# Kernel optimization log

Measured on AMD Instinct MI355X. Metric: run time of the kernel, lower is better.

## Reference

```python
import jax, jax.numpy as jnp
import numpy as np

K = 12  # kNN neighbors (includes self, as in PyG knn(x, x, k))
EPS = 1e-5


def bn(h, g, b):
    # Training-mode BatchNorm over all axes except the last (feature) axis.
    ax = tuple(range(h.ndim - 1))
    m = h.mean(axis=ax, keepdims=True)
    v = h.var(axis=ax, keepdims=True)  # biased variance, as BN uses
    return g * (h - m) * jax.lax.rsqrt(v + EPS) + b


def edge_conv(x, W1, b1, g, be, W2, b2):
    # x: [B, N, C] -> [B, N, H]. Dynamic kNN graph in feature space per graph.
    d2 = jnp.sum(x * x, axis=-1)                                  # [B, N]
    dist = d2[:, :, None] + d2[:, None, :] - 2.0 * jnp.einsum('bic,bjc->bij', x, x)
    _, idx = jax.lax.top_k(-dist, K)                              # [B, N, K]
    xj = jnp.take_along_axis(x[:, None, :, :], idx[:, :, :, None], axis=2)  # [B,N,K,C]
    xi = jnp.broadcast_to(x[:, :, None, :], xj.shape)
    e = jnp.concatenate([xi, xj - xi], axis=-1)                   # [B,N,K,2C]
    h = jax.nn.relu(bn(jnp.einsum('bnkc,ch->bnkh', e, W1) + b1, g, be))
    h = jnp.einsum('bnkh,ho->bnko', h, W2) + b2
    return h.mean(axis=2)                                         # mean aggr over K


def setup_inputs() -> dict:
    key = jax.random.key(0)
    ks = jax.random.split(key, 8)
    B, N, C, H, Hf, O = 32, 1024, 3, 64, 32, 2
    s = 0.1
    return {
        'x': jax.random.normal(ks[0], (B, N, C), jnp.float32),
        'w0a': jax.random.normal(ks[1], (2 * C, H), jnp.float32) * s,
        'b0a': jnp.zeros((H,), jnp.float32),
        'g0': jnp.ones((H,), jnp.float32),
        'be0': jnp.zeros((H,), jnp.float32),
        'w0b': jax.random.normal(ks[2], (H, H), jnp.float32) * s,
        'b0b': jnp.zeros((H,), jnp.float32),
        'wa': jax.random.normal(ks[3], (3, 2 * H, H), jnp.float32) * s,
        'ba': jnp.zeros((3, H), jnp.float32),
        'ga': jnp.ones((3, H), jnp.float32),
        'bea': jnp.zeros((3, H), jnp.float32),
        'wb': jax.random.normal(ks[4], (3, H, H), jnp.float32) * s,
        'bb': jnp.zeros((3, H), jnp.float32),
        'wf1': jax.random.normal(ks[5], (H, Hf), jnp.float32) * s,
        'bf1': jnp.zeros((Hf,), jnp.float32),
        'gf': jnp.ones((Hf,), jnp.float32),
        'bef': jnp.zeros((Hf,), jnp.float32),
        'wf2': jax.random.normal(ks[6], (Hf, O), jnp.float32) * s,
        'bf2': jnp.zeros((O,), jnp.float32),
    }


def reference(x, w0a, b0a, g0, be0, w0b, b0b, wa, ba, ga, bea, wb, bb,
              wf1, bf1, gf, bef, wf2, bf2):
    # Layer 0: input channels = 3
    h = edge_conv(x, w0a, b0a, g0, be0, w0b, b0b)
    # Layers 1..3: input channels = hidden
    for i in range(3):
        h = edge_conv(h, wa[i], ba[i], ga[i], bea[i], wb[i], bb[i])
    pooled = h.mean(axis=1)  # global_mean_pool over nodes -> [B, H]
    z = jax.nn.relu(bn(pooled @ wf1 + bf1, gf, bef))
    return z @ wf2 + bf2     # [B, 2]
```

## Files before the change

### kernel.cpp

```cpp
#include <hip/hip_runtime.h>
#include <cstddef>

#define BATCH 32
#define NPTS  1024
#define K_NN  12
#define HID   64
#define BN_EPS 1e-5f

typedef short bf16x8 __attribute__((ext_vector_type(8)));
typedef float f32x4 __attribute__((ext_vector_type(4)));

template<int C>
__global__ __launch_bounds__(256) void d2_kernel(const float* __restrict__ x,
                                                 float* __restrict__ d2) {
  int gid = blockIdx.x * 256 + threadIdx.x;
  const float* xp = x + (size_t)gid * C;
  float s = 0.f;
#pragma unroll
  for (int c = 0; c < C; ++c) { float v = xp[c]; s = fmaf(v, v, s); }
  d2[gid] = s;
}

__device__ __forceinline__ unsigned long long dkey(float dval, int j) {
  int di = __float_as_int(dval);
  unsigned m = (unsigned)(di >> 31) | 0x80000000u;
  unsigned u = (unsigned)di ^ m;
  return ((unsigned long long)u << 32) | (unsigned)j;
}

__device__ __forceinline__ void cas_u64(unsigned long long &a, unsigned long long &b) {
  unsigned long long x = a, y = b;
  bool c = y < x;
  a = c ? y : x;
  b = c ? x : y;
}

__device__ __forceinline__ void sort16_u64(unsigned long long (&k)[16]) {
  cas_u64(k[0],k[1]);  cas_u64(k[2],k[3]);  cas_u64(k[4],k[5]);  cas_u64(k[6],k[7]);
  cas_u64(k[8],k[9]);  cas_u64(k[10],k[11]); cas_u64(k[12],k[13]); cas_u64(k[14],k[15]);
  cas_u64(k[0],k[2]);  cas_u64(k[1],k[3]);  cas_u64(k[4],k[6]);  cas_u64(k[5],k[7]);
  cas_u64(k[8],k[10]); cas_u64(k[9],k[11]); cas_u64(k[12],k[14]); cas_u64(k[13],k[15]);
  cas_u64(k[1],k[2]);  cas_u64(k[5],k[6]);  cas_u64(k[9],k[10]); cas_u64(k[13],k[14]);
  cas_u64(k[0],k[4]);  cas_u64(k[1],k[5]);  cas_u64(k[2],k[6]);  cas_u64(k[3],k[7]);
  cas_u64(k[8],k[12]); cas_u64(k[9],k[13]); cas_u64(k[10],k[14]); cas_u64(k[11],k[15]);
  cas_u64(k[2],k[4]);  cas_u64(k[3],k[5]);  cas_u64(k[10],k[12]); cas_u64(k[11],k[13]);
  cas_u64(k[1],k[2]);  cas_u64(k[3],k[4]);  cas_u64(k[5],k[6]);
  cas_u64(k[9],k[10]); cas_u64(k[11],k[12]); cas_u64(k[13],k[14]);
  cas_u64(k[0],k[8]);  cas_u64(k[1],k[9]);  cas_u64(k[2],k[10]); cas_u64(k[3],k[11]);
  cas_u64(k[4],k[12]); cas_u64(k[5],k[13]); cas_u64(k[6],k[14]); cas_u64(k[7],k[15]);
  cas_u64(k[4],k[8]);  cas_u64(k[5],k[9]);  cas_u64(k[6],k[10]); cas_u64(k[7],k[11]);
  cas_u64(k[2],k[4]);  cas_u64(k[3],k[5]);  cas_u64(k[6],k[8]);  cas_u64(k[7],k[9]);
  cas_u64(k[10],k[12]); cas_u64(k[11],k[13]);
  cas_u64(k[1],k[2]);  cas_u64(k[3],k[4]);  cas_u64(k[5],k[6]);  cas_u64(k[7],k[8]);
  cas_u64(k[9],k[10]); cas_u64(k[11],k[12]); cas_u64(k[13],k[14]);
}

__device__ __forceinline__ void merge12_u64(unsigned long long (&L)[12],
                                            const unsigned long long* S) {
#pragma unroll
  for (int i = 0; i < 12; ++i) {
    unsigned long long s = S[11 - i];
    L[i] = L[i] < s ? L[i] : s;
  }
  cas_u64(L[0],L[8]);  cas_u64(L[1],L[9]);  cas_u64(L[2],L[10]); cas_u64(L[3],L[11]);
  cas_u64(L[4],L[8]);  cas_u64(L[5],L[9]);  cas_u64(L[6],L[10]); cas_u64(L[7],L[11]);
  cas_u64(L[0],L[2]);  cas_u64(L[1],L[3]);  cas_u64(L[4],L[6]);  cas_u64(L[5],L[7]);
  cas_u64(L[8],L[10]); cas_u64(L[9],L[11]);
  cas_u64(L[0],L[1]);  cas_u64(L[2],L[3]);  cas_u64(L[4],L[5]);  cas_u64(L[6],L[7]);
  cas_u64(L[8],L[9]);  cas_u64(L[10],L[11]);
}

__global__ __launch_bounds__(512, 2) void knn64_mfma_kernel(
    const unsigned short* __restrict__ xh, const unsigned short* __restrict__ xm,
    const unsigned short* __restrict__ xl, const float* __restrict__ d2,
    int* __restrict__ idx,
    const float* __restrict__ hxi, const float* __restrict__ hxj,
    float* __restrict__ partial) {
  const int b    = blockIdx.y;
  const int lane = threadIdx.x & 63;
  const int wv_u = __builtin_amdgcn_readfirstlane(threadIdx.x >> 6);
  const int i0   = blockIdx.x * 64;
  const size_t bbase = (size_t)b * NPTS;
  const float* d2b = d2 + bbase;

  constexpr int NE = 8 * K_NN;
  __shared__ __align__(16) char smem[60416];
  unsigned short* alds = (unsigned short*)smem;
  float* slab = (float*)(smem + 25600 + wv_u * 4352);
  unsigned long long* lk = (unsigned long long*)smem;
  int* jlds = (int*)(smem + 49664);
  float* red1 = (float*)smem;
  float* red2 = (float*)(smem + 2048);

  const int qr = lane >> 4;
  const int lr = lane & 15;

  for (int it = threadIdx.x; it < 1536; it += 512) {
    const int row = it / 24, rem = it % 24, pl = rem >> 3, seg = rem & 7;
    const unsigned short* src = (pl == 0) ? xh : ((pl == 1) ? xm : xl);
    *(bf16x8*)(alds + row * 200 + pl * 64 + seg * 8) =
        *(const bf16x8*)(src + (bbase + i0 + row) * HID + seg * 8);
  }
  __syncthreads();

  unsigned long long L[K_NN];
#pragma unroll
  for (int k = 0; k < K_NN; ++k) L[k] = ~0ULL;

  const int j0 = wv_u * 128;

  bf16x8 Bh0, Bh1, Bm0, Bm1, Bl0, Bl1;
  {
    const size_t brow = (bbase + j0 + lr) * HID;
    Bh0 = *(const bf16x8*)(xh + brow + 0  + qr * 8);
    Bh1 = *(const bf16x8*)(xh + brow + 32 + qr * 8);
    Bm0 = *(const bf16x8*)(xm + brow + 0  + qr * 8);
    Bm1 = *(const bf16x8*)(xm + brow + 32 + qr * 8);
    Bl0 = *(const bf16x8*)(xl + brow + 0  + qr * 8);
    Bl1 = *(const bf16x8*)(xl + brow + 32 + qr * 8);
  }

#pragma unroll 1
  for (int chunk = 0; chunk < 8; ++chunk) {
    const int jb = j0 + chunk * 16;
    const bf16x8 bh0 = Bh0, bh1 = Bh1, bm0 = Bm0, bm1 = Bm1, bl0 = Bl0, bl1 = Bl1;

    f32x4 acc[4];
#pragma unroll
    for (int isub = 0; isub < 4; ++isub) acc[isub] = f32x4{0.f, 0.f, 0.f, 0.f};

#pragma unroll
    for (int isub = 0; isub < 4; ++isub) {
      const int ar = (isub * 16 + lr) * 200;
      bf16x8 Ah0 = *(const bf16x8*)(alds + ar + 0   + qr * 8);
      bf16x8 Ah1 = *(const bf16x8*)(alds + ar + 32  + qr * 8);
      bf16x8 Am0 = *(const bf16x8*)(alds + ar + 64  + qr * 8);
      bf16x8 Am1 = *(const bf16x8*)(alds + ar + 96  + qr * 8);
      bf16x8 Al0 = *(const bf16x8*)(alds + ar + 128 + qr * 8);
      bf16x8 Al1 = *(const bf16x8*)(alds + ar + 160 + qr * 8);
      f32x4 a = acc[isub];
      a = __builtin_amdgcn_mfma_f32_16x16x32_bf16(Ah0, bh0, a, 0, 0, 0);
      a = __builtin_amdgcn_mfma_f32_16x16x32_bf16(Ah1, bh1, a, 0, 0, 0);
      a = __builtin_amdgcn_mfma_f32_16x16x32_bf16(Ah0, bm0, a, 0, 0, 0);
      a = __builtin_amdgcn_mfma_f32_16x16x32_bf16(Ah1, bm1, a, 0, 0, 0);
      a = __builtin_amdgcn_mfma_f32_16x16x32_bf16(Am0, bh0, a, 0, 0, 0);
      a = __builtin_amdgcn_mfma_f32_16x16x32_bf16(Am1, bh1, a, 0, 0, 0);
      a = __builtin_amdgcn_mfma_f32_16x16x32_bf16(Ah0, bl0, a, 0, 0, 0);
      a = __builtin_amdgcn_mfma_f32_16x16x32_bf16(Ah1, bl1, a, 0, 0, 0);
      a = __builtin_amdgcn_mfma_f32_16x16x32_bf16(Al0, bh0, a, 0, 0, 0);
      a = __builtin_amdgcn_mfma_f32_16x16x32_bf16(Al1, bh1, a, 0, 0, 0);
      a = __builtin_amdgcn_mfma_f32_16x16x32_bf16(Am0, bm0, a, 0, 0, 0);
      a = __builtin_amdgcn_mfma_f32_16x16x32_bf16(Am1, bm1, a, 0, 0, 0);
      acc[isub] = a;
    }

    if (chunk < 7) {
      const size_t nrow = (bbase + jb + 16 + lr) * HID;
      Bh0 = *(const bf16x8*)(xh + nrow + 0  + qr * 8);
      Bh1 = *(const bf16x8*)(xh + nrow + 32 + qr * 8);
      Bm0 = *(const bf16x8*)(xm + nrow + 0  + qr * 8);
      Bm1 = *(const bf16x8*)(xm + nrow + 32 + qr * 8);
      Bl0 = *(const bf16x8*)(xl + nrow + 0  + qr * 8);
      Bl1 = *(const bf16x8*)(xl + nrow + 32 + qr * 8);
    }

#pragma unroll
    for (int isub = 0; isub < 4; ++isub)
#pragma unroll
      for (int r = 0; r < 4; ++r)
        slab[(isub * 16 + qr * 4 + r) * 17 + lr] = acc[isub][r];

    unsigned long long S[16];
#pragma unroll
    for (int jj = 0; jj < 16; ++jj) {
      const int j = jb + jj;
      const float dot = slab[lane * 17 + jj];
      const float dval = fmaf(-2.f, dot, d2b[j]);
      S[jj] = dkey(dval, j);
    }
    sort16_u64(S);
    merge12_u64(L, S);
  }

  __syncthreads();
#pragma unroll
  for (int k = 0; k < K_NN; ++k)
    lk[lane * (NE + 1) + wv_u * K_NN + k] = L[k];
  __syncthreads();

  unsigned long long Lm[K_NN];
  if (wv_u < 2) {
    if (wv_u == 0) {
#pragma unroll
      for (int k = 0; k < K_NN; ++k) Lm[k] = L[k];
    } else {
#pragma unroll
      for (int k = 0; k < K_NN; ++k) Lm[k] = lk[lane * (NE + 1) + 4 * K_NN + k];
    }
#pragma unroll 1
    for (int w = 1; w < 4; ++w) {
      unsigned long long M[K_NN];
#pragma unroll
      for (int k = 0; k < K_NN; ++k)
        M[k] = lk[lane * (NE + 1) + (wv_u * 4 + w) * K_NN + k];
      merge12_u64(Lm, M);
    }
  }
  __syncthreads();
  if (wv_u == 1) {
#pragma unroll
    for (int k = 0; k < K_NN; ++k) lk[lane * (NE + 1) + 4 * K_NN + k] = Lm[k];
  }
  __syncthreads();
  if (wv_u == 0) {
    unsigned long long M[K_NN];
#pragma unroll
    for (int k = 0; k < K_NN; ++k) M[k] = lk[lane * (NE + 1) + 4 * K_NN + k];
    merge12_u64(Lm, M);
    int* op = idx + ((size_t)b * NPTS + i0 + lane) * K_NN;
#pragma unroll
    for (int k = 0; k < K_NN; ++k) {
      int jv = (int)(unsigned)(Lm[k] & 0xFFFFFFFFu);
      op[k] = jv;
      jlds[lane * K_NN + k] = jv;
    }
  }
  __syncthreads();

  {
    const float* hxib = hxi + (bbase + i0) * HID;
    const float* hxjb = hxj + bbase * HID;
    float s1 = 0.f, s2 = 0.f;
#pragma unroll 1
    for (int t = 0; t < 8; ++t) {
      const int nl = wv_u * 8 + t;
      const float hv = hxib[(size_t)nl * HID + lane];
      int jj[K_NN];
#pragma unroll
      for (int k = 0; k < K_NN; ++k) jj[k] = jlds[nl * K_NN + k];
      float v[K_NN];
#pragma unroll
      for (int k = 0; k < K_NN; ++k) v[k] = hxjb[(size_t)jj[k] * HID + lane];
#pragma unroll
      for (int k = 0; k < K_NN; ++k) {
        float h = hv + v[k];
        s1 += h;
        s2 = fmaf(h, h, s2);
      }
    }
    red1[wv_u * HID + lane] = s1;
    red2[wv_u * HID + lane] = s2;
  }
  __syncthreads();
  if (threadIdx.x < 128) {
    const int f = threadIdx.x & 63;
    const float* r = (threadIdx.x < 64) ? red1 : red2;
    float a = 0.f;
#pragma unroll
    for (int w = 0; w < 8; ++w) a += r[w * HID + f];
    partial[((size_t)b * 16 + blockIdx.x) * 128 + threadIdx.x] = a;
  }
}

__global__ __launch_bounds__(512, 2) void knn3_kernel(
    const float* __restrict__ x, const float* __restrict__ d2,
    int* __restrict__ idx,
    const float* __restrict__ hxi, const float* __restrict__ hxj,
    float* __restrict__ partial) {
  const int b    = blockIdx.y;
  const int lane = threadIdx.x & 63;
  const int wv_u = __builtin_amdgcn_readfirstlane(threadIdx.x >> 6);
  const int i0   = blockIdx.x * 64;
  const int i    = i0 + lane;
  const size_t bbase = (size_t)b * NPTS;
  const float* xb  = x  + bbase * 3;
  const float* d2b = d2 + bbase;

  constexpr int NE = 8 * K_NN;
  __shared__ __align__(16) char smem[53248];
  unsigned long long* lk = (unsigned long long*)smem;
  int* jlds = (int*)(smem + 49664);
  float* red1 = (float*)smem;
  float* red2 = (float*)(smem + 2048);

  float xi0 = xb[(size_t)i * 3 + 0];
  float xi1 = xb[(size_t)i * 3 + 1];
  float xi2v = xb[(size_t)i * 3 + 2];

  unsigned long long L[K_NN];
#pragma unroll
  for (int k = 0; k < K_NN; ++k) L[k] = ~0ULL;

  const int j0 = wv_u * 128;
#pragma unroll 1
  for (int ch = 0; ch < 8; ++ch) {
    unsigned long long S[16];
#pragma unroll
    for (int jj = 0; jj < 16; ++jj) {
      const int j = j0 + ch * 16 + jj;
      const float* xj = xb + (size_t)j * 3;
      const float d2j = d2b[j];
      float dot = fmaf(xi0, xj[0], 0.f);
      dot = fmaf(xi1, xj[1], dot);
      dot = fmaf(xi2v, xj[2], dot);
      S[jj] = dkey(fmaf(-2.f, dot, d2j), j);
    }
    sort16_u64(S);
    merge12_u64(L, S);
  }

#pragma unroll
  for (int k = 0; k < K_NN; ++k)
    lk[lane * (NE + 1) + wv_u * K_NN + k] = L[k];
  __syncthreads();

  unsigned long long Lm[K_NN];
  if (wv_u < 2) {
    if (wv_u == 0) {
#pragma unroll
      for (int k = 0; k < K_NN; ++k) Lm[k] = L[k];
    } else {
#pragma unroll
      for (int k = 0; k < K_NN; ++k) Lm[k] = lk[lane * (NE + 1) + 4 * K_NN + k];
    }
#pragma unroll 1
    for (int w = 1; w < 4; ++w) {
      unsigned long long M[K_NN];
#pragma unroll
      for (int k = 0; k < K_NN; ++k)
        M[k] = lk[lane * (NE + 1) + (wv_u * 4 + w) * K_NN + k];
      merge12_u64(Lm, M);
    }
  }
  __syncthreads();
  if (wv_u == 1) {
#pragma unroll
    for (int k = 0; k < K_NN; ++k) lk[lane * (NE + 1) + 4 * K_NN + k] = Lm[k];
  }
  __syncthreads();
  if (wv_u == 0) {
    unsigned long long M[K_NN];
#pragma unroll
    for (int k = 0; k < K_NN; ++k) M[k] = lk[lane * (NE + 1) + 4 * K_NN + k];
    merge12_u64(Lm, M);
    int* op = idx + ((size_t)b * NPTS + i0 + lane) * K_NN;
#pragma unroll
    for (int k = 0; k < K_NN; ++k) {
      int jv = (int)(unsigned)(Lm[k] & 0xFFFFFFFFu);
      op[k] = jv;
      jlds[lane * K_NN + k] = jv;
    }
  }
  __syncthreads();

  {
    const float* hxib = hxi + (bbase + i0) * HID;
    const float* hxjb2 = hxj + bbase * HID;
    float s1 = 0.f, s2 = 0.f;
#pragma unroll 1
    for (int t = 0; t < 8; ++t) {
      const int nl = wv_u * 8 + t;
      const float hv = hxib[(size_t)nl * HID + lane];
      int jj[K_NN];
#pragma unroll
      for (int k = 0; k < K_NN; ++k) jj[k] = jlds[nl * K_NN + k];
      float v[K_NN];
#pragma unroll
      for (int k = 0; k < K_NN; ++k) v[k] = hxjb2[(size_t)jj[k] * HID + lane];
#pragma unroll
      for (int k = 0; k < K_NN; ++k) {
        float h = hv + v[k];
        s1 += h;
        s2 = fmaf(h, h, s2);
      }
    }
    red1[wv_u * HID + lane] = s1;
    red2[wv_u * HID + lane] = s2;
  }
  __syncthreads();
  if (threadIdx.x < 128) {
    const int f = threadIdx.x & 63;
    const float* r = (threadIdx.x < 64) ? red1 : red2;
    float a = 0.f;
#pragma unroll
    for (int w = 0; w < 8; ++w) a += r[w * HID + f];
    partial[((size_t)b * 16 + blockIdx.x) * 128 + threadIdx.x] = a;
  }
}

__global__ __launch_bounds__(256) void rowgemm2_kernel(
    const float* __restrict__ X, const float* __restrict__ waL,
    const float* __restrict__ biasA,
    float* __restrict__ YA, float* __restrict__ YB) {
  __shared__ float wsa[HID * HID];
  __shared__ float wsb[HID * HID];
  for (int t = threadIdx.x; t < HID * HID; t += 256) {
    float wbv = waL[4096 + t];
    wsa[t] = waL[t] - wbv;
    wsb[t] = wbv;
  }
  __syncthreads();

  const int lane = threadIdx.x & 63;
  const int wv   = threadIdx.x >> 6;
  const int fq   = lane & 15;
  const int rg   = lane >> 4;
  const int r0   = blockIdx.x * 32 + wv * 8 + rg * 2;

  const float4* X4 = (const float4*)X;
  const float4* WA4 = (const float4*)wsa;
  const float4* WB4 = (const float4*)wsb;
  float aA0[4] = {0,0,0,0}, aA1[4] = {0,0,0,0};
  float aB0[4] = {0,0,0,0}, aB1[4] = {0,0,0,0};

#pragma unroll 2
  for (int cq = 0; cq < 16; ++cq) {
    float4 xa = X4[(size_t)r0 * 16 + cq];
    float4 xb_ = X4[(size_t)(r0 + 1) * 16 + cq];
    float ea[4] = {xa.x, xa.y, xa.z, xa.w};
    float eb[4] = {xb_.x, xb_.y, xb_.z, xb_.w};
#pragma unroll
    for (int d = 0; d < 4; ++d) {
      float4 wa4 = WA4[(cq * 4 + d) * 16 + fq];
      float4 wb4 = WB4[(cq * 4 + d) * 16 + fq];
      float wA[4] = {wa4.x, wa4.y, wa4.z, wa4.w};
      float wB[4] = {wb4.x, wb4.y, wb4.z, wb4.w};
#pragma unroll
      for (int k = 0; k < 4; ++k) {
        aA0[k] = fmaf(ea[d], wA[k], aA0[k]);
        aA1[k] = fmaf(eb[d], wA[k], aA1[k]);
        aB0[k] = fmaf(ea[d], wB[k], aB0[k]);
        aB1[k] = fmaf(eb[d], wB[k], aB1[k]);
      }
    }
  }
  float4 b4 = ((const float4*)biasA)[fq];
  float4 oA0{aA0[0] + b4.x, aA0[1] + b4.y, aA0[2] + b4.z, aA0[3] + b4.w};
  float4 oA1{aA1[0] + b4.x, aA1[1] + b4.y, aA1[2] + b4.z, aA1[3] + b4.w};
  float4 oB0{aB0[0], aB0[1], aB0[2], aB0[3]};
  float4 oB1{aB1[0], aB1[1], aB1[2], aB1[3]};
  ((float4*)YA)[(size_t)r0 * 16 + fq] = oA0;
  ((float4*)YA)[(size_t)(r0 + 1) * 16 + fq] = oA1;
  ((float4*)YB)[(size_t)r0 * 16 + fq] = oB0;
  ((float4*)YB)[(size_t)(r0 + 1) * 16 + fq] = oB1;
}

__global__ __launch_bounds__(256) void dual3_kernel(
    const float* __restrict__ x, const float* __restrict__ w0a,
    const float* __restrict__ b1,
    float* __restrict__ hxi, float* __restrict__ hxj) {
  __shared__ float Cs[3 * HID], Bs[3 * HID], bs[HID];
  for (int t = threadIdx.x; t < 3 * HID; t += 256) {
    float bv = w0a[192 + t];
    Cs[t] = w0a[t] - bv;
    Bs[t] = bv;
  }
  if (threadIdx.x < HID) bs[threadIdx.x] = b1[threadIdx.x];
  __syncthreads();

  const int lane = threadIdx.x & 63;
  const int wv   = __builtin_amdgcn_readfirstlane(threadIdx.x >> 6);
  const int node0 = blockIdx.x * 32;
#pragma unroll 1
  for (int it = 0; it < 8; ++it) {
    const int n = node0 + it * 4 + wv;
    const float* xr = x + (size_t)n * 3;
    float x0 = xr[0], x1 = xr[1], x2 = xr[2];
    float hi = bs[lane];
    hi = fmaf(x0, Cs[0 * HID + lane], hi);
    hi = fmaf(x1, Cs[1 * HID + lane], hi);
    hi = fmaf(x2, Cs[2 * HID + lane], hi);
    float hj = x0 * Bs[0 * HID + lane];
    hj = fmaf(x1, Bs[1 * HID + lane], hj);
    hj = fmaf(x2, Bs[2 * HID + lane], hj);
    hxi[(size_t)n * HID + lane] = hi;
    hxj[(size_t)n * HID + lane] = hj;
  }
}

__global__ __launch_bounds__(512) void bn_reduce_finalize_kernel(
    const float* __restrict__ g, const float* __restrict__ be,
    const float* __restrict__ partial, float* __restrict__ stats) {
  const int t   = threadIdx.x & 127;
  const int grp = threadIdx.x >> 7;
  float a0 = 0.f, a1 = 0.f, a2 = 0.f, a3 = 0.f;
  const int gb0 = grp * 128;
  for (int gb = gb0; gb < gb0 + 128; gb += 4) {
    a0 += partial[(size_t)(gb + 0) * 128 + t];
    a1 += partial[(size_t)(gb + 1) * 128 + t];
    a2 += partial[(size_t)(gb + 2) * 128 + t];
    a3 += partial[(size_t)(gb + 3) * 128 + t];
  }
  __shared__ float sm[4][128];
  sm[grp][t] = (a0 + a1) + (a2 + a3);
  __syncthreads();
  if (threadIdx.x < 128)
    sm[0][t] = (sm[0][t] + sm[1][t]) + (sm[2][t] + sm[3][t]);
  __syncthreads();
  if (threadIdx.x < HID) {
    const float inv_n = 1.f / (float)(BATCH * NPTS * K_NN);
    float m = sm[0][t] * inv_n;
    float v = sm[0][HID + t] * inv_n - m * m;
    float A = g[t] * rsqrtf(v + BN_EPS);
    stats[128 + t] = A;
    stats[192 + t] = be[t] - m * A;
  }
}

__global__ __launch_bounds__(256) void egapply_gemm_kernel(
    const int* __restrict__ idx, const float* __restrict__ hxi,
    const float* __restrict__ hxj, const float* __restrict__ stats,
    const float* __restrict__ W2, const float* __restrict__ b2,
    float* __restrict__ out, float* __restrict__ d2out,
    unsigned short* __restrict__ xsh, unsigned short* __restrict__ xsm,
    unsigned short* __restrict__ xsl) {
  __shared__ float w2s[HID * HID];
  __shared__ float red[32][HID];
  for (int t = threadIdx.x; t < HID * HID; t += 256) w2s[t] = W2[t];

  const int lane = threadIdx.x & 63;
  const int wv   = __builtin_amdgcn_readfirstlane(threadIdx.x >> 6);
  const int node0 = blockIdx.x * 32;
  const float A = stats[128 + lane], Bc = stats[192 + lane];

#pragma unroll 1
  for (int it = 0; it < 4; ++it) {
    const int n0 = node0 + it * 8 + wv;
    const int n1 = n0 + 4;
    const int bbase = (n0 >> 10) << 10;
    const int* ip0 = idx + (size_t)n0 * K_NN;
    const int* ip1 = idx + (size_t)n1 * K_NN;
    int j0[K_NN], j1[K_NN];
#pragma unroll
    for (int k = 0; k < K_NN; ++k) { j0[k] = ip0[k]; j1[k] = ip1[k]; }
    const float hv0 = hxi[(size_t)n0 * HID + lane];
    const float hv1 = hxi[(size_t)n1 * HID + lane];
    float v0[K_NN], v1[K_NN];
#pragma unroll
    for (int k = 0; k < K_NN; ++k) {
      v0[k] = hxj[(size_t)(bbase + j0[k]) * HID + lane];
      v1[k] = hxj[(size_t)(bbase + j1[k]) * HID + lane];
    }
    float a0 = 0.f, a1 = 0.f;
#pragma unroll
    for (int k = 0; k < K_NN; ++k) {
      a0 += fmaxf(fmaf(A, hv0 + v0[k], Bc), 0.f);
      a1 += fmaxf(fmaf(A, hv1 + v1[k], Bc), 0.f);
    }
    red[it * 8 + wv][lane] = a0;
    red[it * 8 + 4 + wv][lane] = a1;
  }
  __syncthreads();

  const float b2f = b2[lane];
  const float inv = 1.f / (float)K_NN;
#pragma unroll 2
  for (int p = 0; p < 8; ++p) {
    int rr = p * 4 + wv;
    float acc = 0.f;
#pragma unroll 8
    for (int h = 0; h < HID; ++h) acc = fmaf(red[rr][h], w2s[h * HID + lane], acc);
    float val = fmaf(acc, inv, b2f);
    const size_t o = (size_t)(node0 + rr) * HID + lane;
    out[o] = val;

    unsigned u = __float_as_uint(val);
    unsigned short hh = (unsigned short)((u + 0x7FFFu + ((u >> 16) & 1u)) >> 16);
    float r1 = val - __uint_as_float((unsigned)hh << 16);
    unsigned ur = __float_as_uint(r1);
    unsigned short mm = (unsigned short)((ur + 0x7FFFu + ((ur >> 16) & 1u)) >> 16);
    float r2 = r1 - __uint_as_float((unsigned)mm << 16);
    unsigned ur2 = __float_as_uint(r2);
    unsigned short ll = (unsigned short)((ur2 + 0x7FFFu + ((ur2 >> 16) & 1u)) >> 16);
    xsh[o] = hh; xsm[o] = mm; xsl[o] = ll;

    float sq = val * val;
#pragma unroll
    for (int off = 1; off < 64; off <<= 1) sq += __shfl_xor(sq, off, 64);
    if (lane == 0) d2out[node0 + rr] = sq;
  }
}

__global__ __launch_bounds__(256) void pool_kernel(const float* __restrict__ h,
                                                   float* __restrict__ pooled) {
  const int b = blockIdx.x;
  const int f = threadIdx.x & 63;
  const int gsz = threadIdx.x >> 6;
  __shared__ float red[4][HID];
  float s = 0.f;
  for (int n = gsz; n < NPTS; n += 4) s += h[((size_t)b * NPTS + n) * HID + f];
  red[gsz][f] = s;
  __syncthreads();
  if (threadIdx.x < HID)
    pooled[b * HID + f] = ((red[0][f] + red[1][f]) + (red[2][f] + red[3][f])) * (1.f / (float)NPTS);
}

__global__ __launch_bounds__(256) void head_kernel(const float* __restrict__ pooled,
    const float* __restrict__ wf1, const float* __restrict__ bf1,
    const float* __restrict__ gf, const float* __restrict__ bef,
    const float* __restrict__ wf2, const float* __restrict__ bf2,
    float* __restrict__ out) {
  __shared__ float pl[BATCH * HID];
  __shared__ float t[BATCH * 32];
  __shared__ float Ab[32], Bb[32];
  for (int i = threadIdx.x; i < BATCH * HID; i += 256) pl[i] = pooled[i];
  __syncthreads();
  for (int i = threadIdx.x; i < BATCH * 32; i += 256) {
    int s = i >> 5, f1 = i & 31;
    float acc = bf1[f1];
    for (int h = 0; h < HID; ++h) acc = fmaf(pl[s * HID + h], wf1[h * 32 + f1], acc);
    t[i] = acc;
  }
  __syncthreads();
  if (threadIdx.x < 32) {
    int f1 = threadIdx.x;
    float m = 0.f;
    for (int s = 0; s < BATCH; ++s) m += t[s * 32 + f1];
    m *= (1.f / (float)BATCH);
    float v = 0.f;
    for (int s = 0; s < BATCH; ++s) { float d = t[s * 32 + f1] - m; v = fmaf(d, d, v); }
    v *= (1.f / (float)BATCH);
    float A = gf[f1] * rsqrtf(v + BN_EPS);
    Ab[f1] = A; Bb[f1] = bef[f1] - m * A;
  }
  __syncthreads();
  for (int i = threadIdx.x; i < BATCH * 32; i += 256) {
    int f1 = i & 31;
    t[i] = fmaxf(fmaf(Ab[f1], t[i], Bb[f1]), 0.f);
  }
  __syncthreads();
  if (threadIdx.x < BATCH * 2) {
    int s = threadIdx.x >> 1, o = threadIdx.x & 1;
    float acc = bf2[o];
    for (int f1 = 0; f1 < 32; ++f1) acc = fmaf(t[s * 32 + f1], wf2[f1 * 2 + o], acc);
    out[s * 2 + o] = acc;
  }
}

extern "C" void kernel_launch(void* const* d_in, const int* in_sizes, int n_in,
                              void* d_out, int out_size, void* d_ws, size_t ws_size,
                              hipStream_t stream) {
  const float* x   = (const float*)d_in[0];
  const float* w0a = (const float*)d_in[1];
  const float* b0a = (const float*)d_in[2];
  const float* g0  = (const float*)d_in[3];
  const float* be0 = (const float*)d_in[4];
  const float* w0b = (const float*)d_in[5];
  const float* b0b = (const float*)d_in[6];
  const float* wa  = (const float*)d_in[7];
  const float* ba  = (const float*)d_in[8];
  const float* ga  = (const float*)d_in[9];
  const float* bea = (const float*)d_in[10];
  const float* wb  = (const float*)d_in[11];
  const float* bb  = (const float*)d_in[12];
  const float* wf1 = (const float*)d_in[13];
  const float* bf1 = (const float*)d_in[14];
  const float* gf  = (const float*)d_in[15];
  const float* bef = (const float*)d_in[16];
  const float* wf2 = (const float*)d_in[17];
  const float* bf2 = (const float*)d_in[18];

  float* ws = (float*)d_ws;
  const size_t HN = (size_t)BATCH * NPTS * HID;
  const size_t ROWS = (size_t)BATCH * NPTS;
  float* bufA    = ws;
  float* bufB    = bufA + HN;
  float* hxi     = bufB + HN;
  float* hxjb    = hxi + HN;
  int*   idxb    = (int*)(hxjb + HN);
  float* d2buf   = (float*)(idxb + ROWS * K_NN);
  float* stats   = d2buf + ROWS;
  float* partial = stats + 256;
  float* pooled  = partial + 1024 * 128;
  unsigned short* xsh = (unsigned short*)(pooled + 2048);
  unsigned short* xsm = xsh + HN;
  unsigned short* xsl = xsm + HN;

  d2_kernel<3><<<(int)(ROWS / 256), 256, 0, stream>>>(x, d2buf);
  dual3_kernel<<<1024, 256, 0, stream>>>(x, w0a, b0a, hxi, hxjb);
  knn3_kernel<<<dim3(16, BATCH), 512, 0, stream>>>(x, d2buf, idxb, hxi, hxjb, partial);
  bn_reduce_finalize_kernel<<<1, 512, 0, stream>>>(g0, be0, partial, stats);
  egapply_gemm_kernel<<<1024, 256, 0, stream>>>(idxb, hxi, hxjb, stats, w0b, b0b,
                                                bufA, d2buf, xsh, xsm, xsl);

  const float* cur = bufA;
  float* nxt = bufB;
  for (int i = 0; i < 3; ++i) {
    rowgemm2_kernel<<<(int)(ROWS / 32), 256, 0, stream>>>(cur, wa + (size_t)i * 8192,
                                                          ba + i * HID, hxi, hxjb);
    knn64_mfma_kernel<<<dim3(16, BATCH), 512, 0, stream>>>(xsh, xsm, xsl, d2buf, idxb,
                                                           hxi, hxjb, partial);
    bn_reduce_finalize_kernel<<<1, 512, 0, stream>>>(ga + i * HID, bea + i * HID, partial, stats);
    egapply_gemm_kernel<<<1024, 256, 0, stream>>>(idxb, hxi, hxjb, stats,
                                                  wb + (size_t)i * 4096, bb + i * HID,
                                                  nxt, d2buf, xsh, xsm, xsl);
    const float* t = cur; cur = nxt; nxt = (float*)t;
  }

  pool_kernel<<<BATCH, 256, 0, stream>>>(cur, pooled);
  head_kernel<<<1, 256, 0, stream>>>(pooled, wf1, bf1, gf, bef, wf2, bf2, (float*)d_out);
}
```

Before: 580.0 us.

## Software-pipeline kNN MFMA with top-k scan and split merges into 8-wide sorts

Restructures the kNN distance loop into two-chunk ping-pong stages. The MFMA tile for the next 16 columns is issued before the previous chunk's slab results are scanned and merged, so matrix-core work can overlap the VALU sorting. The 16-element sort plus merge is replaced by two 8-element sorting networks, each merged into the running top-12 list through the same bitonic step, which cuts compare-and-swap count. The cost is more live registers (two B-operand sets), which could increase spilling or pressure at the 512-thread, 2-block launch bounds.

After: 650.5 us. +12.1%, slower.

```diff
diff --git a/kernel.cpp b/kernel.cpp
--- a/kernel.cpp
+++ b/kernel.cpp
@@ -55,19 +55,42 @@
   cas_u64(k[9],k[10]); cas_u64(k[11],k[12]); cas_u64(k[13],k[14]);
 }
 
-__device__ __forceinline__ void merge12_u64(unsigned long long (&L)[12],
-                                            const unsigned long long* S) {
-#pragma unroll
-  for (int i = 0; i < 12; ++i) {
-    unsigned long long s = S[11 - i];
-    L[i] = L[i] < s ? L[i] : s;
-  }
+__device__ __forceinline__ void sort8_u64(unsigned long long (&k)[8]) {
+  cas_u64(k[0],k[1]); cas_u64(k[2],k[3]); cas_u64(k[4],k[5]); cas_u64(k[6],k[7]);
+  cas_u64(k[0],k[2]); cas_u64(k[1],k[3]); cas_u64(k[4],k[6]); cas_u64(k[5],k[7]);
+  cas_u64(k[1],k[2]); cas_u64(k[5],k[6]);
+  cas_u64(k[0],k[4]); cas_u64(k[1],k[5]); cas_u64(k[2],k[6]); cas_u64(k[3],k[7]);
+  cas_u64(k[2],k[4]); cas_u64(k[3],k[5]);
+  cas_u64(k[1],k[2]); cas_u64(k[3],k[4]); cas_u64(k[5],k[6]);
+}
+
+__device__ __forceinline__ void bitonic12_u64(unsigned long long (&L)[12]) {
   cas_u64(L[0],L[8]);  cas_u64(L[1],L[9]);  cas_u64(L[2],L[10]); cas_u64(L[3],L[11]);
   cas_u64(L[4],L[8]);  cas_u64(L[5],L[9]);  cas_u64(L[6],L[10]); cas_u64(L[7],L[11]);
   cas_u64(L[0],L[2]);  cas_u64(L[1],L[3]);  cas_u64(L[4],L[6]);  cas_u64(L[5],L[7]);
   cas_u64(L[8],L[10]); cas_u64(L[9],L[11]);
   cas_u64(L[0],L[1]);  cas_u64(L[2],L[3]);  cas_u64(L[4],L[5]);  cas_u64(L[6],L[7]);
   cas_u64(L[8],L[9]);  cas_u64(L[10],L[11]);
+}
+
+__device__ __forceinline__ void merge12_u64(unsigned long long (&L)[12],
+                                            const unsigned long long* S) {
+#pragma unroll
+  for (int i = 0; i < 12; ++i) {
+    unsigned long long s = S[11 - i];
+    L[i] = L[i] < s ? L[i] : s;
+  }
+  bitonic12_u64(L);
+}
+
+__device__ __forceinline__ void merge8_12_u64(unsigned long long (&L)[12],
+                                              const unsigned long long (&S)[8]) {
+#pragma unroll
+  for (int i = 4; i < 12; ++i) {
+    unsigned long long s = S[11 - i];
+    L[i] = L[i] < s ? L[i] : s;
+  }
+  bitonic12_u64(L);
 }
 
 __global__ __launch_bounds__(512, 2) void knn64_mfma_kernel(
@@ -109,78 +132,94 @@
 
   const int j0 = wv_u * 128;
 
-  bf16x8 Bh0, Bh1, Bm0, Bm1, Bl0, Bl1;
-  {
-    const size_t brow = (bbase + j0 + lr) * HID;
-    Bh0 = *(const bf16x8*)(xh + brow + 0  + qr * 8);
-    Bh1 = *(const bf16x8*)(xh + brow + 32 + qr * 8);
-    Bm0 = *(const bf16x8*)(xm + brow + 0  + qr * 8);
-    Bm1 = *(const bf16x8*)(xm + brow + 32 + qr * 8);
-    Bl0 = *(const bf16x8*)(xl + brow + 0  + qr * 8);
-    Bl1 = *(const bf16x8*)(xl + brow + 32 + qr * 8);
-  }
+#define KNN64_MFMA_PHASE(BH0, BH1, BM0, BM1, BL0, BL1)                        \
+  _Pragma("unroll")                                                           \
+  for (int isub = 0; isub < 4; ++isub) {                                      \
+    const int ar = (isub * 16 + lr) * 200;                                    \
+    bf16x8 Ah0 = *(const bf16x8*)(alds + ar + 0   + qr * 8);                  \
+    bf16x8 Ah1 = *(const bf16x8*)(alds + ar + 32  + qr * 8);                  \
+    bf16x8 Am0 = *(const bf16x8*)(alds + ar + 64  + qr * 8);                  \
+    bf16x8 Am1 = *(const bf16x8*)(alds + ar + 96  + qr * 8);                  \
+    bf16x8 Al0 = *(const bf16x8*)(alds + ar + 128 + qr * 8);                  \
+    bf16x8 Al1 = *(const bf16x8*)(alds + ar + 160 + qr * 8);                  \
+    f32x4 a = f32x4{0.f, 0.f, 0.f, 0.f};                                      \
+    a = __builtin_amdgcn_mfma_f32_16x16x32_bf16(Ah0, BH0, a, 0, 0, 0);        \
+    a = __builtin_amdgcn_mfma_f32_16x16x32_bf16(Ah1, BH1, a, 0, 0, 0);        \
+    a = __builtin_amdgcn_mfma_f32_16x16x32_bf16(Ah0, BM0, a, 0, 0, 0);        \
+    a = __builtin_amdgcn_mfma_f32_16x16x32_bf16(Ah1, BM1, a, 0, 0, 0);        \
+    a = __builtin_amdgcn_mfma_f32_16x16x32_bf16(Am0, BH0, a, 0, 0, 0);        \
+    a = __builtin_amdgcn_mfma_f32_16x16x32_bf16(Am1, BH1, a, 0, 0, 0);        \
+    a = __builtin_amdgcn_mfma_f32_16x16x32_bf16(Ah0, BL0, a, 0, 0, 0);        \
+    a = __builtin_amdgcn_mfma_f32_16x16x32_bf16(Ah1, BL1, a, 0, 0, 0);        \
+    a = __builtin_amdgcn_mfma_f32_16x16x32_bf16(Al0, BH0, a, 0, 0, 0);        \
+    a = __builtin_amdgcn_mfma_f32_16x16x32_bf16(Al1, BH1, a, 0, 0, 0);        \
+    a = __builtin_amdgcn_mfma_f32_16x16x32_bf16(Am0, BM0, a, 0, 0, 0);        \
+    a = __builtin_amdgcn_mfma_f32_16x16x32_bf16(Am1, BM1, a, 0, 0, 0);        \
+    acc[isub] = a;                                                            \
+  }
+
+#define KNN64_SLAB_WRITE()                                                    \
+  _Pragma("unroll")                                                           \
+  for (int isub = 0; isub < 4; ++isub)                                        \
+    _Pragma("unroll")                                                         \
+    for (int r = 0; r < 4; ++r)                                               \
+      slab[(isub * 16 + qr * 4 + r) * 17 + lr] = acc[isub][r];
+
+#define KNN64_SCAN(JP)                                                        \
+  {                                                                           \
+    const int jp_ = (JP);                                                     \
+    unsigned long long S[8];                                                  \
+    _Pragma("unroll")                                                         \
+    for (int t = 0; t < 8; ++t) {                                             \
+      const float dot = slab[lane * 17 + t];                                  \
+      S[t] = dkey(fmaf(-2.f, dot, d2b[jp_ + t]), jp_ + t);                    \
+    }                                                                         \
+    sort8_u64(S);                                                             \
+    merge8_12_u64(L, S);                                                      \
+    _Pragma("unroll")                                                         \
+    for (int t = 0; t < 8; ++t) {                                             \
+      const float dot = slab[lane * 17 + 8 + t];                              \
+      S[t] = dkey(fmaf(-2.f, dot, d2b[jp_ + 8 + t]), jp_ + 8 + t);            \
+    }                                                                         \
+    sort8_u64(S);                                                             \
+    merge8_12_u64(L, S);                                                      \
+  }
+
+#define KNN64_LOAD_B(H0, H1, M0, M1, L0, L1, JROW)                            \
+  {                                                                           \
+    const size_t brow_ = (bbase + (JROW) + lr) * HID;                         \
+    H0 = *(const bf16x8*)(xh + brow_ + 0  + qr * 8);                          \
+    H1 = *(const bf16x8*)(xh + brow_ + 32 + qr * 8);                          \
+    M0 = *(const bf16x8*)(xm + brow_ + 0  + qr * 8);                          \
+    M1 = *(const bf16x8*)(xm + brow_ + 32 + qr * 8);                          \
+    L0 = *(const bf16x8*)(xl + brow_ + 0  + qr * 8);                          \
+    L1 = *(const bf16x8*)(xl + brow_ + 32 + qr * 8);                          \
+  }
+
+  bf16x8 B0h0, B0h1, B0m0, B0m1, B0l0, B0l1;
+  bf16x8 B1h0, B1h1, B1m0, B1m1, B1l0, B1l1;
+  KNN64_LOAD_B(B0h0, B0h1, B0m0, B0m1, B0l0, B0l1, j0);
+
+  f32x4 acc[4];
 
 #pragma unroll 1
-  for (int chunk = 0; chunk < 8; ++chunk) {
-    const int jb = j0 + chunk * 16;
-    const bf16x8 bh0 = Bh0, bh1 = Bh1, bm0 = Bm0, bm1 = Bm1, bl0 = Bl0, bl1 = Bl1;
-
-    f32x4 acc[4];
-#pragma unroll
-    for (int isub = 0; isub < 4; ++isub) acc[isub] = f32x4{0.f, 0.f, 0.f, 0.f};
-
-#pragma unroll
-    for (int isub = 0; isub < 4; ++isub) {
-      const int ar = (isub * 16 + lr) * 200;
-      bf16x8 Ah0 = *(const bf16x8*)(alds + ar + 0   + qr * 8);
-      bf16x8 Ah1 = *(const bf16x8*)(alds + ar + 32  + qr * 8);
-      bf16x8 Am0 = *(const bf16x8*)(alds + ar + 64  + qr * 8);
-      bf16x8 Am1 = *(const bf16x8*)(alds + ar + 96  + qr * 8);
-      bf16x8 Al0 = *(const bf16x8*)(alds + ar + 128 + qr * 8);
-      bf16x8 Al1 = *(const bf16x8*)(alds + ar + 160 + qr * 8);
-      f32x4 a = acc[isub];
-      a = __builtin_amdgcn_mfma_f32_16x16x32_bf16(Ah0, bh0, a, 0, 0, 0);
-      a = __builtin_amdgcn_mfma_f32_16x16x32_bf16(Ah1, bh1, a, 0, 0, 0);
-      a = __builtin_amdgcn_mfma_f32_16x16x32_bf16(Ah0, bm0, a, 0, 0, 0);
-      a = __builtin_amdgcn_mfma_f32_16x16x32_bf16(Ah1, bm1, a, 0, 0, 0);
-      a = __builtin_amdgcn_mfma_f32_16x16x32_bf16(Am0, bh0, a, 0, 0, 0);
-      a = __builtin_amdgcn_mfma_f32_16x16x32_bf16(Am1, bh1, a, 0, 0, 0);
-      a = __builtin_amdgcn_mfma_f32_16x16x32_bf16(Ah0, bl0, a, 0, 0, 0);
-      a = __builtin_amdgcn_mfma_f32_16x16x32_bf16(Ah1, bl1, a, 0, 0, 0);
-      a = __builtin_amdgcn_mfma_f32_16x16x32_bf16(Al0, bh0, a, 0, 0, 0);
-      a = __builtin_amdgcn_mfma_f32_16x16x32_bf16(Al1, bh1, a, 0, 0, 0);
-      a = __builtin_amdgcn_mfma_f32_16x16x32_bf16(Am0, bm0, a, 0, 0, 0);
-      a = __builtin_amdgcn_mfma_f32_16x16x32_bf16(Am1, bm1, a, 0, 0, 0);
-      acc[isub] = a;
-    }
-
-    if (chunk < 7) {
-      const size_t nrow = (bbase + jb + 16 + lr) * HID;
-      Bh0 = *(const bf16x8*)(xh + nrow + 0  + qr * 8);
-      Bh1 = *(const bf16x8*)(xh + nrow + 32 + qr * 8);
-      Bm0 = *(const bf16x8*)(xm + nrow + 0  + qr * 8);
-      Bm1 = *(const bf16x8*)(xm + nrow + 32 + qr * 8);
-      Bl0 = *(const bf16x8*)(xl + nrow + 0  + qr * 8);
-      Bl1 = *(const bf16x8*)(xl + nrow + 32 + qr * 8);
-    }
-
-#pragma unroll
-    for (int isub = 0; isub < 4; ++isub)
-#pragma unroll
-      for (int r = 0; r < 4; ++r)
-        slab[(isub * 16 + qr * 4 + r) * 17 + lr] = acc[isub][r];
-
-    unsigned long long S[16];
-#pragma unroll
-    for (int jj = 0; jj < 16; ++jj) {
-      const int j = jb + jj;
-      const float dot = slab[lane * 17 + jj];
-      const float dval = fmaf(-2.f, dot, d2b[j]);
-      S[jj] = dkey(dval, j);
-    }
-    sort16_u64(S);
-    merge12_u64(L, S);
-  }
+  for (int cc = 0; cc < 4; ++cc) {
+    const int ce = cc * 2;
+    KNN64_MFMA_PHASE(B0h0, B0h1, B0m0, B0m1, B0l0, B0l1)
+    KNN64_LOAD_B(B1h0, B1h1, B1m0, B1m1, B1l0, B1l1, j0 + (ce + 1) * 16)
+    if (ce > 0) KNN64_SCAN(j0 + (ce - 1) * 16)
+    KNN64_SLAB_WRITE()
+    KNN64_MFMA_PHASE(B1h0, B1h1, B1m0, B1m1, B1l0, B1l1)
+    if (cc < 3) KNN64_LOAD_B(B0h0, B0h1, B0m0, B0m1, B0l0, B0l1, j0 + (ce + 2) * 16)
+    KNN64_SCAN(j0 + ce * 16)
+    KNN64_SLAB_WRITE()
+  }
+  KNN64_SCAN(j0 + 112)
+
+#undef KNN64_MFMA_PHASE
+#undef KNN64_SLAB_WRITE
+#undef KNN64_SCAN
+#undef KNN64_LOAD_B
 
   __syncthreads();
 #pragma unroll
```
